# Kernel tuning notes

Hardware: AMD Instinct MI355X
Metric: run time of the kernel (lower is better)

Reference implementation:

```python
import jax, jax.numpy as jnp
import numpy as np

NUM_HEADS = 4
D_MODEL = 256
HEAD_DIM = D_MODEL // NUM_HEADS  # 64
B, N = 8, 2048


def _proj(x, W, b):
    # Conv1d with kernel_size=1 == pointwise linear over channel dim
    # x: [B, C_in, N], W: [C_out, C_in], b: [C_out]
    return jnp.einsum('oi,bin->bon', W, x) + b[None, :, None]


def setup_inputs() -> dict:
    key = jax.random.key(0)
    ks = jax.random.split(key, 11)
    s = 1.0 / np.sqrt(D_MODEL)
    return {
        'query': jax.random.normal(ks[0], (B, D_MODEL, N), jnp.float32),
        'key':   jax.random.normal(ks[1], (B, D_MODEL, N), jnp.float32),
        'value': jax.random.normal(ks[2], (B, D_MODEL, N), jnp.float32),
        'Wq': jax.random.normal(ks[3], (D_MODEL, D_MODEL), jnp.float32) * s,
        'bq': jax.random.normal(ks[4], (D_MODEL,), jnp.float32) * 0.01,
        'Wk': jax.random.normal(ks[5], (D_MODEL, D_MODEL), jnp.float32) * s,
        'bk': jax.random.normal(ks[6], (D_MODEL,), jnp.float32) * 0.01,
        'Wv': jax.random.normal(ks[7], (D_MODEL, D_MODEL), jnp.float32) * s,
        'bv': jax.random.normal(ks[8], (D_MODEL,), jnp.float32) * 0.01,
        'Wm': jax.random.normal(ks[9], (D_MODEL, D_MODEL), jnp.float32) * s,
        'bm': jax.random.normal(ks[10], (D_MODEL,), jnp.float32) * 0.01,
    }


def reference(query, key, value, Wq, bq, Wk, bk, Wv, bv, Wm, bm):
    b = query.shape[0]
    # project then split channels into (head_dim, num_heads): [B, d, h, N]
    q = _proj(query, Wq, bq).reshape(b, HEAD_DIM, NUM_HEADS, -1)
    k = _proj(key,   Wk, bk).reshape(b, HEAD_DIM, NUM_HEADS, -1)
    v = _proj(value, Wv, bv).reshape(b, HEAD_DIM, NUM_HEADS, -1)
    scale = 1.0 / jnp.sqrt(jnp.asarray(HEAD_DIM, q.dtype))
    scores = jnp.einsum('bdhn,bdhm->bhnm', q, k) * scale  # [B,H,N,N]
    prob = jax.nn.softmax(scores, axis=-1)
    x = jnp.einsum('bhnm,bdhm->bdhn', prob, v)  # [B,d,H,N]
    x = x.reshape(b, HEAD_DIM * NUM_HEADS, -1)  # [B, d_model, N]
    return _proj(x, Wm, bm)
```

## Files before the change

### kernel.cpp

```cpp
#include <hip/hip_runtime.h>
#include <math.h>


constexpr int BATCH  = 8;
constexpr int DMODEL = 256;
constexpr int SEQ    = 2048;
constexpr int HDIM   = 64;
constexpr int TN     = 128;
constexpr int TM     = 64;
constexpr int NJT    = SEQ / TM;

typedef _Float16 half2_t __attribute__((ext_vector_type(2)));
typedef _Float16 half4_t __attribute__((ext_vector_type(4)));
typedef _Float16 half8_t __attribute__((ext_vector_type(8)));
typedef float    float4_t __attribute__((ext_vector_type(4)));

static __device__ __forceinline__ void ld16_lds(const void* g, void* l) {
    __builtin_amdgcn_global_load_lds(
        (const __attribute__((address_space(1))) unsigned*)g,
        (__attribute__((address_space(3))) unsigned*)l, 16, 0, 0);
}

static __device__ __forceinline__ half8_t cvt8(const float4 w0, const float4 w1) {
    half8_t a;
    a[0] = (_Float16)w0.x; a[1] = (_Float16)w0.y;
    a[2] = (_Float16)w0.z; a[3] = (_Float16)w0.w;
    a[4] = (_Float16)w1.x; a[5] = (_Float16)w1.y;
    a[6] = (_Float16)w1.z; a[7] = (_Float16)w1.w;
    return a;
}

__global__ __launch_bounds__(256, 3)
void gemm_qkv(const float* __restrict__ Wq, const float* __restrict__ Wk,
              const float* __restrict__ Wv, const float* __restrict__ Wm,
              const float* __restrict__ bq, const float* __restrict__ bk,
              const float* __restrict__ bv,
              const float* __restrict__ Xq, const float* __restrict__ Xk,
              const float* __restrict__ Xv, _Float16* __restrict__ qT,
              _Float16* __restrict__ kT, _Float16* __restrict__ vT,
              _Float16* __restrict__ wfp)
{
    if (blockIdx.y == 24) {
        const int r = blockIdx.x * 8 + (threadIdx.x >> 5);
        const int c32 = threadIdx.x & 31;
        half8_t o8;
        #pragma unroll
        for (int e = 0; e < 8; ++e) {
            const int hd = c32 * 8 + e;
            o8[e] = (_Float16)Wm[r * DMODEL + 4 * (hd & 63) + (hd >> 6)];
        }
        *(half8_t*)&wfp[(size_t)r * DMODEL + c32 * 8] = o8;
        return;
    }

    const int n0 = blockIdx.x * 64;
    const int proj = blockIdx.y >> 3, b = blockIdx.y & 7;
    const float* W    = proj == 0 ? Wq : proj == 1 ? Wk : Wv;
    const float* bias = proj == 0 ? bq : proj == 1 ? bk : bv;
    const float* X    = (proj == 0 ? Xq : proj == 1 ? Xk : Xv)
                        + (size_t)b * DMODEL * SEQ;
    const float qs = (proj == 0) ? 0.18033688011112042f : 1.0f;

    __shared__ __align__(16) char lds[50432];
    float*    T  = (float*)lds;
    _Float16* Xs = (_Float16*)(lds + 16640);
    _Float16* Tw = (_Float16*)lds;

    const int tid = threadIdx.x, tn = tid & 15, tc = tid >> 4;

    #pragma unroll
    for (int cc = 0; cc < 4; ++cc) {
        __syncthreads();
        #pragma unroll
        for (int i = 0; i < 4; ++i) {
            const int c = tc + 16 * i;
            const float4 v = *(const float4*)&X[(size_t)(cc * 64 + c) * SEQ + n0 + tn * 4];
            T[c * 65 + tn * 4 + 0] = v.x; T[c * 65 + tn * 4 + 1] = v.y;
            T[c * 65 + tn * 4 + 2] = v.z; T[c * 65 + tn * 4 + 3] = v.w;
        }
        __syncthreads();
        #pragma unroll
        for (int i = 0; i < 4; ++i) {
            const int n = tc + 16 * i;
            half4_t h4;
            #pragma unroll
            for (int j = 0; j < 4; ++j) h4[j] = (_Float16)T[(tn * 4 + j) * 65 + n];
            *(half4_t*)&Xs[n * 264 + cc * 64 + tn * 4] = h4;
        }
    }
    __syncthreads();

    const int w = tid >> 6, lane = tid & 63;
    const int lm = lane & 15, g = lane >> 4, g8 = g * 8;
    const int cw0 = w * 64;

    float4_t acc[4][4];
    #pragma unroll
    for (int mt = 0; mt < 4; ++mt)
        #pragma unroll
        for (int nt = 0; nt < 4; ++nt) acc[mt][nt] = (float4_t){0.f, 0.f, 0.f, 0.f};

    #pragma unroll
    for (int k0 = 0; k0 < DMODEL; k0 += 64) {
        half8_t a[4][2], bb[4][2];
        #pragma unroll
        for (int mt = 0; mt < 4; ++mt)
            #pragma unroll
            for (int kd = 0; kd < 2; ++kd) {
                const float* wp = &W[(size_t)(cw0 + mt * 16 + lm) * DMODEL
                                     + k0 + kd * 32 + g8];
                a[mt][kd] = cvt8(*(const float4*)wp, *(const float4*)(wp + 4));
            }
        #pragma unroll
        for (int nt = 0; nt < 4; ++nt)
            #pragma unroll
            for (int kd = 0; kd < 2; ++kd)
                bb[nt][kd] = *(const half8_t*)&Xs[(nt * 16 + lm) * 264
                                                  + k0 + kd * 32 + g8];
        #pragma unroll
        for (int kd = 0; kd < 2; ++kd)
            #pragma unroll
            for (int mt = 0; mt < 4; ++mt)
                #pragma unroll
                for (int nt = 0; nt < 4; ++nt)
                    acc[mt][nt] = __builtin_amdgcn_mfma_f32_16x16x32_f16(
                        a[mt][kd], bb[nt][kd], acc[mt][nt], 0, 0, 0);
    }
    __syncthreads();

    #pragma unroll
    for (int mt = 0; mt < 4; ++mt) {
        const float4 b4 = *(const float4*)&bias[cw0 + mt * 16 + g * 4];
        const float bb4[4] = {b4.x, b4.y, b4.z, b4.w};
        #pragma unroll
        for (int nt = 0; nt < 4; ++nt) {
            half4_t pk;
            #pragma unroll
            for (int r = 0; r < 4; ++r)
                pk[r] = (_Float16)((acc[mt][nt][r] + bb4[r]) * qs);
            *(half4_t*)&Tw[((w * 64 + nt * 16 + lm)) * 68 + mt * 16 + g * 4] = pk;
        }
    }
    __syncthreads();

    if (proj < 2) {
        _Float16* dst = (proj == 0 ? qT : kT);
        const int h = w;
        const int dcg = lane & 7, nlb = lane >> 3;
        #pragma unroll
        for (int it = 0; it < 8; ++it) {
            const int nl = it * 8 + nlb;
            const int hs = (nl & 3) | (((nl >> 3) & 1) << 2);
            half8_t ch;
            #pragma unroll
            for (int e = 0; e < 8; ++e) {
                ch[e] = Tw[((dcg >> 1) * 64 + nl) * 68
                           + 4 * ((dcg & 1) * 8 + e) + h];
            }
            const int chunk = dcg ^ hs;
            *(half8_t*)&dst[((size_t)(b * 4 + h) * SEQ + n0 + nl) * HDIM
                            + chunk * 8] = ch;
        }
    } else {
        const int h = w;
        const int jc = lane & 7, db = lane >> 3;
        const size_t tilebase =
            (((size_t)(b * 4 + h) * NJT + (n0 >> 6)) * HDIM) * (size_t)TM;
        #pragma unroll
        for (int it = 0; it < 8; ++it) {
            const int d = it * 8 + db;
            half8_t ch;
            #pragma unroll
            for (int e = 0; e < 8; ++e) {
                ch[e] = Tw[((d >> 4) * 64 + jc * 8 + e) * 68
                           + 4 * (d & 15) + h];
            }
            *(half8_t*)&vT[tilebase + (size_t)d * TM + ((jc ^ (d & 7)) << 3)] = ch;
        }
    }
}

__global__ __launch_bounds__(256, 4)
void attn_f16(const _Float16* __restrict__ qT, const _Float16* __restrict__ kT,
              const _Float16* __restrict__ vT, _Float16* __restrict__ xa,
              _Float16* __restrict__ xb, float* __restrict__ rs)
{
    const int lid = blockIdx.x;
    const int work = (lid & 7) * 128 + (lid >> 3);
    const int bh = work >> 5, b = bh >> 2, h = bh & 3;
    const int jh = (work >> 4) & 1;
    const int ib = work & 15;
    const int tid = threadIdx.x, wid = tid >> 6, lane = tid & 63;
    const int lm = lane & 15, g = lane >> 4;
    const int i0 = ib * TN + wid * 32;

    __shared__ _Float16 Kb[2][TM * HDIM];
    __shared__ _Float16 Vb[2][TM * HDIM];

    const int hq = (lm & 3) | (((lm >> 3) & 1) << 2);
    const int hk = (lm & 3) | (((lm >> 2) & 1) << 2);
    const int rbase = 8 * (lm >> 2) + (lm & 3);

    half8_t bq[2][2];
    const _Float16* qbase = qT + (size_t)bh * SEQ * HDIM;
    #pragma unroll
    for (int rt = 0; rt < 2; ++rt)
        #pragma unroll
        for (int kd = 0; kd < 2; ++kd) {
            const int row = i0 + rt * 16 + lm;
            bq[rt][kd] = *(const half8_t*)(qbase + (size_t)row * HDIM
                                           + (((kd * 4 + g) ^ hq) << 3));
        }

    const char* kt = (const char*)(kT + ((size_t)bh * SEQ + jh * (SEQ / 2)) * HDIM);
    const char* vt = (const char*)(vT + ((size_t)bh * NJT + jh * 16) * TM * HDIM);

    float4_t o[2][4];
    float rsum[2][2] = {{0.f, 0.f}, {0.f, 0.f}};
    #pragma unroll
    for (int rt = 0; rt < 2; ++rt)
        #pragma unroll
        for (int dt = 0; dt < 4; ++dt) o[rt][dt] = (float4_t){0.f, 0.f, 0.f, 0.f};

    #define STAGE(jt, bu)                                                     \
        {                                                                     \
            const char* kg = kt + (size_t)(jt) * 8192;                        \
            const char* vg = vt + (size_t)(jt) * 8192;                        \
            _Pragma("unroll")                                                 \
            for (int p = 0; p < 2; ++p) {                                     \
                const int c = wid + p * 4;                                    \
                ld16_lds(kg + c * 1024 + lane * 16, (char*)&Kb[bu][0] + c * 1024); \
                ld16_lds(vg + c * 1024 + lane * 16, (char*)&Vb[bu][0] + c * 1024); \
            }                                                                 \
        }

    STAGE(0, 0);
    __syncthreads();

    for (int jt = 0; jt < 16; ++jt) {
        const int cur = jt & 1;
        if (jt + 1 < 16) STAGE(jt + 1, cur ^ 1);

        float4_t s[2][2][2];
        #pragma unroll
        for (int jb = 0; jb < 2; ++jb)
            #pragma unroll
            for (int u = 0; u < 2; ++u)
                #pragma unroll
                for (int rt = 0; rt < 2; ++rt)
                    s[jb][u][rt] = (float4_t){0.f, 0.f, 0.f, 0.f};
        #pragma unroll
        for (int kd = 0; kd < 2; ++kd)
            #pragma unroll
            for (int jb = 0; jb < 2; ++jb)
                #pragma unroll
                for (int u = 0; u < 2; ++u) {
                    const int jrow = jb * 32 + rbase + 4 * u;
                    const half8_t fk = *(const half8_t*)
                        &Kb[cur][jrow * HDIM + (((kd * 4 + g) ^ hk) << 3)];
                    #pragma unroll
                    for (int rt = 0; rt < 2; ++rt)
                        s[jb][u][rt] = __builtin_amdgcn_mfma_f32_16x16x32_f16(
                            fk, bq[rt][kd], s[jb][u][rt], 0, 0, 0);
                }

        half8_t ap[2][2];
        #pragma unroll
        for (int jb = 0; jb < 2; ++jb)
            #pragma unroll
            for (int rt = 0; rt < 2; ++rt) {
                half8_t p;
                #pragma unroll
                for (int r = 0; r < 4; ++r) {
                    const float e0 = __builtin_amdgcn_exp2f(s[jb][0][rt][r]);
                    const float e1 = __builtin_amdgcn_exp2f(s[jb][1][rt][r]);
                    rsum[jb][rt] += e0;
                    rsum[jb][rt] += e1;
                    p[r]     = (_Float16)e0;
                    p[r + 4] = (_Float16)e1;
                }
                ap[jb][rt] = p;
            }

        #pragma unroll
        for (int jb = 0; jb < 2; ++jb)
            #pragma unroll
            for (int dt = 0; dt < 4; ++dt) {
                const int d = dt * 16 + lm;
                const half8_t fv = *(const half8_t*)
                    &Vb[cur][d * TM + (((jb * 4 + g) ^ (lm & 7)) << 3)];
                #pragma unroll
                for (int rt = 0; rt < 2; ++rt)
                    o[rt][dt] = __builtin_amdgcn_mfma_f32_16x16x32_f16(
                        ap[jb][rt], fv, o[rt][dt], 0, 0, 0);
            }
        __syncthreads();
    }

    _Float16* xp = jh ? xb : xa;
    #pragma unroll
    for (int rt = 0; rt < 2; ++rt)
        #pragma unroll
        for (int dt = 0; dt < 4; ++dt) {
            const int d = dt * 16 + lm;
            #pragma unroll
            for (int r = 0; r < 4; ++r) {
                const int n = i0 + rt * 16 + 4 * g + r;
                xp[((size_t)b * SEQ + n) * DMODEL + h * HDIM + d] =
                    (_Float16)o[rt][dt][r];
            }
        }
    #pragma unroll
    for (int rt = 0; rt < 2; ++rt) {
        float v = rsum[0][rt] + rsum[1][rt];
        v += __shfl_xor(v, 16);
        v += __shfl_xor(v, 32);
        if (g == 0)
            rs[((size_t)jh * 32 + bh) * SEQ + i0 + rt * 16 + lm] = v;
    }
    #undef STAGE
}

__global__ __launch_bounds__(256)
void gemm_final(const _Float16* __restrict__ wfp, const float* __restrict__ bias,
                const _Float16* __restrict__ xa, const _Float16* __restrict__ xb,
                const float* __restrict__ rs, float* __restrict__ out)
{
    const int n0 = blockIdx.x * 64, m0 = blockIdx.y * 128;
    const int b = blockIdx.z;
    const int tid = threadIdx.x, w = tid >> 6, lane = tid & 63;
    const int lm = lane & 15, g = lane >> 4, g8 = g * 8;
    const int cw0 = m0 + w * 32;

    __shared__ _Float16 Xc[64 * DMODEL];

    {
        const int c8 = tid & 31, nb = tid >> 5;
        const _Float16* Pa = xa + ((size_t)b * SEQ + n0) * DMODEL;
        const _Float16* Pb = xb + ((size_t)b * SEQ + n0) * DMODEL;
        #pragma unroll
        for (int j = 0; j < 8; ++j) {
            const int n = nb * 8 + j;
            const size_t off = (size_t)n * DMODEL + c8 * 8;
            const half8_t va = *(const half8_t*)&Pa[off];
            const half8_t vb = *(const half8_t*)&Pb[off];
            const half8_t sv = va + vb;
            *(half8_t*)&Xc[n * DMODEL + ((c8 ^ (n & 7)) << 3)] = sv;
        }
    }

    _Float16 pmh[4][4];
    #pragma unroll
    for (int nt = 0; nt < 4; ++nt) {
        const int n = n0 + nt * 16 + lm;
        #pragma unroll
        for (int hh = 0; hh < 4; ++hh) {
            const float l = rs[(size_t)(b * 4 + hh) * SEQ + n]
                          + rs[(size_t)(32 + b * 4 + hh) * SEQ + n];
            pmh[nt][hh] = (_Float16)(1.0f / l);
        }
    }
    __syncthreads();

    float4_t acc[2][4];
    #pragma unroll
    for (int mt = 0; mt < 2; ++mt)
        #pragma unroll
        for (int nt = 0; nt < 4; ++nt) acc[mt][nt] = (float4_t){0.f, 0.f, 0.f, 0.f};

    #pragma unroll
    for (int k0 = 0; k0 < DMODEL; k0 += 64) {
        half8_t a[2][2], bb[4][2];
        #pragma unroll
        for (int mt = 0; mt < 2; ++mt)
            #pragma unroll
            for (int kd = 0; kd < 2; ++kd)
                a[mt][kd] = *(const half8_t*)&wfp[(size_t)(cw0 + mt * 16 + lm) * DMODEL
                                                  + k0 + kd * 32 + g8];
        #pragma unroll
        for (int nt = 0; nt < 4; ++nt)
            #pragma unroll
            for (int kd = 0; kd < 2; ++kd) {
                const int n = nt * 16 + lm;
                const int c8 = (k0 >> 3) + kd * 4 + g;
                const half8_t sv = *(const half8_t*)
                    &Xc[n * DMODEL + ((c8 ^ (n & 7)) << 3)];
                const int hh = (k0 + kd * 32 + g8) >> 6;
                bb[nt][kd] = sv * pmh[nt][hh];
            }
        #pragma unroll
        for (int kd = 0; kd < 2; ++kd)
            #pragma unroll
            for (int mt = 0; mt < 2; ++mt)
                #pragma unroll
                for (int nt = 0; nt < 4; ++nt)
                    acc[mt][nt] = __builtin_amdgcn_mfma_f32_16x16x32_f16(
                        a[mt][kd], bb[nt][kd], acc[mt][nt], 0, 0, 0);
    }

    #pragma unroll
    for (int mt = 0; mt < 2; ++mt)
        #pragma unroll
        for (int r = 0; r < 4; ++r) {
            const int co = cw0 + mt * 16 + g * 4 + r;
            const float bv_ = bias[co];
            #pragma unroll
            for (int nt = 0; nt < 4; ++nt)
                out[((size_t)b * DMODEL + co) * SEQ + n0 + nt * 16 + lm] =
                    acc[mt][nt][r] + bv_;
        }
}

extern "C" void kernel_launch(void* const* d_in, const int* in_sizes, int n_in,
                              void* d_out, int out_size, void* d_ws, size_t ws_size,
                              hipStream_t stream) {
    const float* query = (const float*)d_in[0];
    const float* key_  = (const float*)d_in[1];
    const float* value = (const float*)d_in[2];
    const float* Wq = (const float*)d_in[3];  const float* bq = (const float*)d_in[4];
    const float* Wk = (const float*)d_in[5];  const float* bk = (const float*)d_in[6];
    const float* Wv = (const float*)d_in[7];  const float* bv = (const float*)d_in[8];
    const float* Wm = (const float*)d_in[9];  const float* bm = (const float*)d_in[10];
    float* out = (float*)d_out;

    const size_t bufElems = (size_t)BATCH * DMODEL * SEQ;
    _Float16* qT = (_Float16*)d_ws;
    _Float16* kT = qT + bufElems;
    _Float16* vT = kT + bufElems;
    _Float16* xa = vT + bufElems;
    _Float16* xb = xa + bufElems;
    float*    rsb = (float*)(xb + bufElems);
    _Float16* wfp = (_Float16*)(rsb + 2 * 32 * SEQ);

    gemm_qkv<<<dim3(SEQ / 64, 25), 256, 0, stream>>>(
        Wq, Wk, Wv, Wm, bq, bk, bv, query, key_, value, qT, kT, vT, wfp);
    attn_f16<<<dim3(1024), 256, 0, stream>>>(qT, kT, vT, xa, xb, rsb);
    gemm_final<<<dim3(SEQ / 64, 2, BATCH), 256, 0, stream>>>(
        wfp, bm, xa, xb, rsb, out);
}
```

Before: 175.3 us.

## Drop split-KV in attention and fuse softmax normalization into attention epilogue

The attention kernel no longer splits the key sequence into two halves. Each block now walks all 32 key tiles and normalizes its output by the row sum before writing a single fp16 buffer. The final projection therefore no longer reads two partial buffers plus row sums and rescales in its inner loop, and its tiling changes to 32 columns by all 256 output channels per block. This cuts the memory traffic and final-GEMM overhead but halves the attention grid to 512 blocks, which may underfill the GPU and lengthen each block's serial loop.

```diff
diff --git a/kernel.cpp b/kernel.cpp
--- a/kernel.cpp
+++ b/kernel.cpp
@@ -6,7 +6,6 @@
 constexpr int DMODEL = 256;
 constexpr int SEQ    = 2048;
 constexpr int HDIM   = 64;
-constexpr int TN     = 128;
 constexpr int TM     = 64;
 constexpr int NJT    = SEQ / TM;
 
@@ -180,19 +179,17 @@
     }
 }
 
-__global__ __launch_bounds__(256, 4)
+__global__ __launch_bounds__(256, 2)
 void attn_f16(const _Float16* __restrict__ qT, const _Float16* __restrict__ kT,
-              const _Float16* __restrict__ vT, _Float16* __restrict__ xa,
-              _Float16* __restrict__ xb, float* __restrict__ rs)
+              const _Float16* __restrict__ vT, _Float16* __restrict__ xp)
 {
     const int lid = blockIdx.x;
-    const int work = (lid & 7) * 128 + (lid >> 3);
-    const int bh = work >> 5, b = bh >> 2, h = bh & 3;
-    const int jh = (work >> 4) & 1;
+    const int work = (lid & 7) * 64 + (lid >> 3);
+    const int bh = work >> 4, b = bh >> 2, h = bh & 3;
     const int ib = work & 15;
     const int tid = threadIdx.x, wid = tid >> 6, lane = tid & 63;
     const int lm = lane & 15, g = lane >> 4;
-    const int i0 = ib * TN + wid * 32;
+    const int i0 = ib * 128 + wid * 32;
 
     __shared__ _Float16 Kb[2][TM * HDIM];
     __shared__ _Float16 Vb[2][TM * HDIM];
@@ -212,8 +209,8 @@
                                            + (((kd * 4 + g) ^ hq) << 3));
         }
 
-    const char* kt = (const char*)(kT + ((size_t)bh * SEQ + jh * (SEQ / 2)) * HDIM);
-    const char* vt = (const char*)(vT + ((size_t)bh * NJT + jh * 16) * TM * HDIM);
+    const char* kt = (const char*)(kT + (size_t)bh * SEQ * HDIM);
+    const char* vt = (const char*)(vT + (size_t)bh * NJT * TM * HDIM);
 
     float4_t o[2][4];
     float rsum[2][2] = {{0.f, 0.f}, {0.f, 0.f}};
@@ -237,9 +234,9 @@
     STAGE(0, 0);
     __syncthreads();
 
-    for (int jt = 0; jt < 16; ++jt) {
+    for (int jt = 0; jt < NJT; ++jt) {
         const int cur = jt & 1;
-        if (jt + 1 < 16) STAGE(jt + 1, cur ^ 1);
+        if (jt + 1 < NJT) STAGE(jt + 1, cur ^ 1);
 
         float4_t s[2][2][2];
         #pragma unroll
@@ -297,115 +294,94 @@
         __syncthreads();
     }
 
-    _Float16* xp = jh ? xb : xa;
-    #pragma unroll
-    for (int rt = 0; rt < 2; ++rt)
-        #pragma unroll
-        for (int dt = 0; dt < 4; ++dt) {
-            const int d = dt * 16 + lm;
-            #pragma unroll
-            for (int r = 0; r < 4; ++r) {
-                const int n = i0 + rt * 16 + 4 * g + r;
-                xp[((size_t)b * SEQ + n) * DMODEL + h * HDIM + d] =
-                    (_Float16)o[rt][dt][r];
-            }
-        }
     #pragma unroll
     for (int rt = 0; rt < 2; ++rt) {
         float v = rsum[0][rt] + rsum[1][rt];
         v += __shfl_xor(v, 16);
         v += __shfl_xor(v, 32);
-        if (g == 0)
-            rs[((size_t)jh * 32 + bh) * SEQ + i0 + rt * 16 + lm] = v;
+        float inv[4];
+        #pragma unroll
+        for (int r = 0; r < 4; ++r)
+            inv[r] = 1.0f / __shfl(v, 4 * g + r);
+        #pragma unroll
+        for (int dt = 0; dt < 4; ++dt) {
+            const int d = dt * 16 + lm;
+            #pragma unroll
+            for (int r = 0; r < 4; ++r) {
+                const int n = i0 + rt * 16 + 4 * g + r;
+                xp[((size_t)b * SEQ + n) * DMODEL + h * HDIM + d] =
+                    (_Float16)(o[rt][dt][r] * inv[r]);
+            }
+        }
     }
     #undef STAGE
 }
 
-__global__ __launch_bounds__(256)
+__global__ __launch_bounds__(256, 3)
 void gemm_final(const _Float16* __restrict__ wfp, const float* __restrict__ bias,
-                const _Float16* __restrict__ xa, const _Float16* __restrict__ xb,
-                const float* __restrict__ rs, float* __restrict__ out)
+                const _Float16* __restrict__ xp, float* __restrict__ out)
 {
-    const int n0 = blockIdx.x * 64, m0 = blockIdx.y * 128;
-    const int b = blockIdx.z;
+    const int n0 = blockIdx.x * 32, b = blockIdx.y;
     const int tid = threadIdx.x, w = tid >> 6, lane = tid & 63;
     const int lm = lane & 15, g = lane >> 4, g8 = g * 8;
-    const int cw0 = m0 + w * 32;
-
-    __shared__ _Float16 Xc[64 * DMODEL];
+    const int cw0 = w * 64;
+
+    __shared__ _Float16 Xc[32 * DMODEL];
 
     {
         const int c8 = tid & 31, nb = tid >> 5;
-        const _Float16* Pa = xa + ((size_t)b * SEQ + n0) * DMODEL;
-        const _Float16* Pb = xb + ((size_t)b * SEQ + n0) * DMODEL;
-        #pragma unroll
-        for (int j = 0; j < 8; ++j) {
-            const int n = nb * 8 + j;
-            const size_t off = (size_t)n * DMODEL + c8 * 8;
-            const half8_t va = *(const half8_t*)&Pa[off];
-            const half8_t vb = *(const half8_t*)&Pb[off];
-            const half8_t sv = va + vb;
-            *(half8_t*)&Xc[n * DMODEL + ((c8 ^ (n & 7)) << 3)] = sv;
-        }
-    }
-
-    _Float16 pmh[4][4];
-    #pragma unroll
-    for (int nt = 0; nt < 4; ++nt) {
-        const int n = n0 + nt * 16 + lm;
-        #pragma unroll
-        for (int hh = 0; hh < 4; ++hh) {
-            const float l = rs[(size_t)(b * 4 + hh) * SEQ + n]
-                          + rs[(size_t)(32 + b * 4 + hh) * SEQ + n];
-            pmh[nt][hh] = (_Float16)(1.0f / l);
+        const _Float16* P = xp + ((size_t)b * SEQ + n0) * DMODEL;
+        #pragma unroll
+        for (int j = 0; j < 4; ++j) {
+            const int n = nb * 4 + j;
+            const half8_t v = *(const half8_t*)&P[(size_t)n * DMODEL + c8 * 8];
+            *(half8_t*)&Xc[n * DMODEL + ((c8 ^ (n & 7)) << 3)] = v;
         }
     }
     __syncthreads();
 
-    float4_t acc[2][4];
-    #pragma unroll
-    for (int mt = 0; mt < 2; ++mt)
-        #pragma unroll
-        for (int nt = 0; nt < 4; ++nt) acc[mt][nt] = (float4_t){0.f, 0.f, 0.f, 0.f};
+    float4_t acc[4][2];
+    #pragma unroll
+    for (int mt = 0; mt < 4; ++mt)
+        #pragma unroll
+        for (int nt = 0; nt < 2; ++nt) acc[mt][nt] = (float4_t){0.f, 0.f, 0.f, 0.f};
 
     #pragma unroll
     for (int k0 = 0; k0 < DMODEL; k0 += 64) {
-        half8_t a[2][2], bb[4][2];
-        #pragma unroll
-        for (int mt = 0; mt < 2; ++mt)
+        half8_t a[4][2], bb[2][2];
+        #pragma unroll
+        for (int mt = 0; mt < 4; ++mt)
             #pragma unroll
             for (int kd = 0; kd < 2; ++kd)
                 a[mt][kd] = *(const half8_t*)&wfp[(size_t)(cw0 + mt * 16 + lm) * DMODEL
                                                   + k0 + kd * 32 + g8];
         #pragma unroll
-        for (int nt = 0; nt < 4; ++nt)
+        for (int nt = 0; nt < 2; ++nt)
             #pragma unroll
             for (int kd = 0; kd < 2; ++kd) {
                 const int n = nt * 16 + lm;
                 const int c8 = (k0 >> 3) + kd * 4 + g;
-                const half8_t sv = *(const half8_t*)
+                bb[nt][kd] = *(const half8_t*)
                     &Xc[n * DMODEL + ((c8 ^ (n & 7)) << 3)];
-                const int hh = (k0 + kd * 32 + g8) >> 6;
-                bb[nt][kd] = sv * pmh[nt][hh];
             }
         #pragma unroll
         for (int kd = 0; kd < 2; ++kd)
             #pragma unroll
-            for (int mt = 0; mt < 2; ++mt)
-                #pragma unroll
-                for (int nt = 0; nt < 4; ++nt)
+            for (int mt = 0; mt < 4; ++mt)
+                #pragma unroll
+                for (int nt = 0; nt < 2; ++nt)
                     acc[mt][nt] = __builtin_amdgcn_mfma_f32_16x16x32_f16(
                         a[mt][kd], bb[nt][kd], acc[mt][nt], 0, 0, 0);
     }
 
     #pragma unroll
-    for (int mt = 0; mt < 2; ++mt)
+    for (int mt = 0; mt < 4; ++mt)
         #pragma unroll
         for (int r = 0; r < 4; ++r) {
             const int co = cw0 + mt * 16 + g * 4 + r;
             const float bv_ = bias[co];
             #pragma unroll
-            for (int nt = 0; nt < 4; ++nt)
+            for (int nt = 0; nt < 2; ++nt)
                 out[((size_t)b * DMODEL + co) * SEQ + n0 + nt * 16 + lm] =
                     acc[mt][nt][r] + bv_;
         }
@@ -427,14 +403,12 @@
     _Float16* qT = (_Float16*)d_ws;
     _Float16* kT = qT + bufElems;
     _Float16* vT = kT + bufElems;
-    _Float16* xa = vT + bufElems;
-    _Float16* xb = xa + bufElems;
-    float*    rsb = (float*)(xb + bufElems);
-    _Float16* wfp = (_Float16*)(rsb + 2 * 32 * SEQ);
+    _Float16* xp = vT + bufElems;
+    _Float16* wfp = xp + bufElems;
 
     gemm_qkv<<<dim3(SEQ / 64, 25), 256, 0, stream>>>(
         Wq, Wk, Wv, Wm, bq, bk, bv, query, key_, value, qT, kT, vT, wfp);
-    attn_f16<<<dim3(1024), 256, 0, stream>>>(qT, kT, vT, xa, xb, rsb);
-    gemm_final<<<dim3(SEQ / 64, 2, BATCH), 256, 0, stream>>>(
-        wfp, bm, xa, xb, rsb, out);
-}
+    attn_f16<<<dim3(512), 256, 0, stream>>>(qT, kT, vT, xp);
+    gemm_final<<<dim3(SEQ / 32, BATCH), 256, 0, stream>>>(
+        wfp, bm, xp, out);
+}
```

After: 178.6 us. Within noise of the previous version (+1.9%).
